# Kernel optimization log

Measured on AMD Instinct MI355X. Metric: run time of the kernel, lower is better.

Reference implementation:

```python
import jax, jax.numpy as jnp
import numpy as np

D_MODEL = 1024
N_SA = 8          # self-attention heads
N_RA = 8          # relational-attention heads
TOTAL = N_SA + N_RA
HEAD_DIM = D_MODEL // TOTAL   # 64
KEY_DIM = HEAD_DIM            # default key_dim = d_model // total_n_heads
N_REL = 8                     # n_relations (= n_heads_ra default)
REL_PROJ = KEY_DIM            # rel_proj_dim default
B, S = 4, 1024


def _rope(x, cos, sin):
    # x: [b, s, h, d]; cos/sin: [s, d//2]; interleaved-pair rotation as in apply_rotary_emb
    xr = x.reshape(x.shape[:-1] + (-1, 2))
    x_r, x_i = xr[..., 0], xr[..., 1]
    c = cos[None, :, None, :]
    s = sin[None, :, None, :]
    o_r = x_r * c - x_i * s
    o_i = x_r * s + x_i * c
    return jnp.stack([o_r, o_i], axis=-1).reshape(x.shape)


def setup_inputs() -> dict:
    key = jax.random.key(0)
    ks = jax.random.split(key, 16)
    def p(k, shape, scale=0.02):
        return jax.random.normal(k, shape, dtype=jnp.float32) * scale
    x = jax.random.normal(ks[0], (B, S, D_MODEL), dtype=jnp.float32)
    symbols = jax.random.normal(ks[1], (B, S, D_MODEL), dtype=jnp.float32)
    # standard RoPE frequency tables, shape [S, KEY_DIM//2]
    inv_freq = 1.0 / (10000.0 ** (np.arange(0, KEY_DIM, 2, dtype=np.float32) / KEY_DIM))
    ang = np.outer(np.arange(S, dtype=np.float32), inv_freq)
    freqs_cos = jnp.asarray(np.cos(ang), dtype=jnp.float32)
    freqs_sin = jnp.asarray(np.sin(ang), dtype=jnp.float32)
    return dict(
        x=x, symbols=symbols, freqs_cos=freqs_cos, freqs_sin=freqs_sin,
        # self-attention stream params
        wq_sa=p(ks[2], (D_MODEL, N_SA * KEY_DIM)),
        wk_sa=p(ks[3], (D_MODEL, N_SA * KEY_DIM)),
        wv_sa=p(ks[4], (D_MODEL, N_SA * HEAD_DIM)),
        wo_sa=p(ks[5], (N_SA * HEAD_DIM, N_SA * HEAD_DIM)),
        # relational-attention stream params
        wq_attn=p(ks[6], (D_MODEL, N_RA * KEY_DIM)),
        wk_attn=p(ks[7], (D_MODEL, N_RA * KEY_DIM)),
        wq_rel=p(ks[8], (D_MODEL, N_REL * REL_PROJ)),
        wk_rel=p(ks[9], (D_MODEL, N_REL * REL_PROJ)),
        wr=p(ks[10], (N_RA, HEAD_DIM, N_REL)),      # per-head relation->head_dim map
        wv_sym=p(ks[11], (D_MODEL, N_RA * HEAD_DIM)),  # symbol projection
        wo_ra=p(ks[12], (N_RA * HEAD_DIM, N_RA * HEAD_DIM)),
    )


def reference(x, symbols, freqs_cos, freqs_sin, wq_sa, wk_sa, wv_sa, wo_sa,
              wq_attn, wk_attn, wq_rel, wk_rel, wr, wv_sym, wo_ra):
    b, s, _ = x.shape
    attn_scale = 1.0 / jnp.sqrt(jnp.asarray(HEAD_DIM, dtype=x.dtype))
    rel_scale = 1.0 / jnp.sqrt(jnp.asarray(REL_PROJ, dtype=x.dtype))
    causal = jnp.tril(jnp.ones((s, s), dtype=bool))
    neg = jnp.where(causal, jnp.asarray(0.0, x.dtype), jnp.asarray(-jnp.inf, x.dtype))

    # ---- standard self-attention stream ----
    q = _rope((x @ wq_sa).reshape(b, s, N_SA, KEY_DIM), freqs_cos, freqs_sin)
    k = _rope((x @ wk_sa).reshape(b, s, N_SA, KEY_DIM), freqs_cos, freqs_sin)
    v = (x @ wv_sa).reshape(b, s, N_SA, HEAD_DIM)
    scores = jnp.einsum('bihd,bjhd->bhij', q, k) * attn_scale + neg
    attn = jax.nn.softmax(scores, axis=-1)
    sa_out = jnp.einsum('bhij,bjhd->bihd', attn, v).reshape(b, s, -1) @ wo_sa

    # ---- relational attention stream ----
    qa = _rope((x @ wq_attn).reshape(b, s, N_RA, KEY_DIM), freqs_cos, freqs_sin)
    ka = _rope((x @ wk_attn).reshape(b, s, N_RA, KEY_DIM), freqs_cos, freqs_sin)
    ra_scores = jnp.einsum('bihd,bjhd->bhij', qa, ka) * attn_scale + neg
    ra_attn = jax.nn.softmax(ra_scores, axis=-1)
    # relations r(i,j) in R^{n_rel}: inner products of relation projections, tanh-activated
    qr = (x @ wq_rel).reshape(b, s, N_REL, REL_PROJ)
    kr = (x @ wk_rel).reshape(b, s, N_REL, REL_PROJ)
    rel = jnp.tanh(jnp.einsum('bird,bjrd->bijr', qr, kr) * rel_scale)  # [b,s,s,n_rel]
    sv = (symbols @ wv_sym).reshape(b, s, N_RA, HEAD_DIM)
    sym_msg = jnp.einsum('bhij,bjhd->bihd', ra_attn, sv)
    rel_msg = jnp.einsum('bhij,bijr->bihr', ra_attn, rel)
    rel_proj = jnp.einsum('bihr,hdr->bihd', rel_msg, wr)
    ra_out = (sym_msg + rel_proj).reshape(b, s, -1) @ wo_ra

    # dual attention: concat the two streams along feature dim -> [b, s, d_model]
    return jnp.concatenate([sa_out, ra_out], axis=-1)
```

## Files before the change

### kernel.cpp

```cpp
#include <hip/hip_runtime.h>

typedef unsigned short u16;
typedef unsigned int u32;
typedef __attribute__((ext_vector_type(8))) short s16x8;
typedef __attribute__((ext_vector_type(4))) float f32x4;

#define C_QSA 0
#define C_KSA 512
#define C_VSA 1024
#define C_QA  1536
#define C_KA  2048
#define C_QR  2560
#define C_KR  3072
#define C_SV  3584
#define LDP   4096

__device__ __forceinline__ u16 f2bf(float f) {
    union { float f; unsigned u; } v; v.f = f;
    return (u16)((v.u + 0x7FFFu + ((v.u >> 16) & 1u)) >> 16);
}
__device__ __forceinline__ float bf2f(u16 h) {
    union { unsigned u; float f; } v; v.u = ((unsigned)h) << 16; return v.f;
}
__device__ __forceinline__ float fexp(float y) {
    return __builtin_exp2f(y * 1.4426950408889634f);
}
__device__ __forceinline__ float ftanh(float x) {
    float e = __builtin_exp2f(x * 2.885390081777927f);
    return 1.f - 2.f / (e + 1.f);
}
__device__ __forceinline__ f32x4 mfma16(s16x8 a, s16x8 b, f32x4 c) {
    return __builtin_amdgcn_mfma_f32_16x16x32_bf16(a, b, c, 0, 0, 0);
}
__device__ __forceinline__ void gload16(const u16* g, u16* l) {
    __builtin_amdgcn_global_load_lds(
        (const __attribute__((address_space(1))) void*)g,
        (__attribute__((address_space(3))) void*)l, 16, 0, 0);
}


__global__ void cvt2_f32_bf16(const float* __restrict__ a, const float* __restrict__ b,
                              u16* __restrict__ oa, u16* __restrict__ ob) {
    int i = (blockIdx.x * 256 + threadIdx.x) * 8;
    const int half = (i >= 4194304) ? 1 : 0;
    const float* in = half ? b : a;
    u16* out = half ? ob : oa;
    int off = i - half * 4194304;
    float4 x = *(const float4*)(in + off);
    float4 y = *(const float4*)(in + off + 4);
    s16x8 o;
    o[0] = (short)f2bf(x.x); o[1] = (short)f2bf(x.y);
    o[2] = (short)f2bf(x.z); o[3] = (short)f2bf(x.w);
    o[4] = (short)f2bf(y.x); o[5] = (short)f2bf(y.y);
    o[6] = (short)f2bf(y.z); o[7] = (short)f2bf(y.w);
    *(s16x8*)(out + off) = o;
}

struct WP { const float* p[10]; };

__global__ void transpose_w(WP wp, u16* __restrict__ WcatT,
                            u16* __restrict__ woSaT, u16* __restrict__ woRaT) {
    const int z = blockIdx.z;
    const float* W;
    u16* Wt;
    int K;
    if (z < 8) { W = wp.p[z]; Wt = WcatT + (size_t)z * 524288; K = 1024; }
    else       { W = wp.p[z]; Wt = (z == 8) ? woSaT : woRaT;   K = 512;  }
    const int N = 512;
    const int kt = blockIdx.x * 32, nt = blockIdx.y * 32;
    if (kt >= K) return;
    __shared__ float t[32][33];
    const int c = threadIdx.x & 31, r0 = threadIdx.x >> 5;
#pragma unroll
    for (int it = 0; it < 4; ++it) {
        int r = it * 8 + r0;
        t[r][c] = W[(size_t)(kt + r) * N + nt + c];
    }
    __syncthreads();
#pragma unroll
    for (int it = 0; it < 4; ++it) {
        int r = it * 8 + r0;
        Wt[(size_t)(nt + r) * K + kt + c] = f2bf(t[c][r]);
    }
}

__global__ void transpose_v2(const u16* __restrict__ P, u16* __restrict__ Vt, int colOff) {
    const int st = blockIdx.x * 32, ht = blockIdx.y * 32, b = blockIdx.z;
    __shared__ u16 t[32][34];
    const int c = threadIdx.x & 31, r0 = threadIdx.x >> 5;
#pragma unroll
    for (int it = 0; it < 4; ++it) {
        int r = it * 8 + r0;
        t[r][c] = P[(size_t)(b * 1024 + st + r) * LDP + colOff + ht + c];
    }
    __syncthreads();
    const int cp = ((c & 15) >> 2) * 8 + (c >> 4) * 4 + (c & 3);
#pragma unroll
    for (int it = 0; it < 4; ++it) {
        int r = it * 8 + r0;
        Vt[(size_t)b * 524288 + (size_t)(ht + r) * 1024 + st + cp] = t[c][r];
    }
}


__global__ void rope_kernel(u16* __restrict__ P, const float* __restrict__ fcos,
                            const float* __restrict__ fsin) {
    int idx = blockIdx.x * 256 + threadIdx.x;
    int row = idx >> 10;
    int rem = idx & 1023;
    int region = rem >> 8;
    int pr = rem & 255;
    int head = pr >> 5, p = pr & 31;
    int off = (region + (region >> 1)) * 512;
    int col = off + head * 64 + 2 * p;
    int s = row & 1023;
    float c = fcos[s * 32 + p], sn = fsin[s * 32 + p];
    u32* ptr = (u32*)(P + (size_t)row * LDP + col);
    u32 v = *ptr;
    float xr = bf2f((u16)(v & 0xffff)), xi = bf2f((u16)(v >> 16));
    u16 o0 = f2bf(xr * c - xi * sn);
    u16 o1 = f2bf(xr * sn + xi * c);
    *ptr = (u32)o0 | ((u32)o1 << 16);
}


template<bool OUT_BF16, bool SWZ>
__global__ __launch_bounds__(256) void gemm_bf16(
    const u16* __restrict__ A, const u16* __restrict__ A2, int lda, int nswitch,
    const u16* __restrict__ Bt, int ldb,
    void* __restrict__ Cp, int ldc, int ccolOff, int K)
{
    __shared__ u16 As[128][64];
    __shared__ u16 Bs[128][64];
    const int tid = threadIdx.x;
    int bx = blockIdx.x, by = blockIdx.y;
    if (SWZ) {
        int lin = by * gridDim.x + bx;
        int k = lin & 7, j = lin >> 3;
        bx = (k & 3) * 8 + (j & 7);
        by = (k >> 2) * 16 + (j >> 3);
    }
    const int m0 = bx * 128, n0 = by * 128;
    const u16* Ause = (A2 != nullptr && n0 >= nswitch) ? A2 : A;
    const int w = tid >> 6, lane = tid & 63;
    const int w32 = w * 32;
    const int wm = (w >> 1) * 64, wn = (w & 1) * 64;
    const int lr = lane & 15, lg = lane >> 4;
    const int srow = lane >> 3;
    const int sc16 = ((lane & 7) ^ srow) * 8;
    f32x4 acc[4][4] = {};

    for (int k0 = 0; k0 < K; k0 += 64) {
        const u16* ga = &Ause[(size_t)(m0 + w32 + srow) * lda + k0 + sc16];
        const u16* gb = &Bt [(size_t)(n0 + w32 + srow) * ldb + k0 + sc16];
        gload16(ga,            &As[w32][0]);
        gload16(ga +  8 * lda, &As[w32 +  8][0]);
        gload16(ga + 16 * lda, &As[w32 + 16][0]);
        gload16(ga + 24 * lda, &As[w32 + 24][0]);
        gload16(gb,            &Bs[w32][0]);
        gload16(gb +  8 * ldb, &Bs[w32 +  8][0]);
        gload16(gb + 16 * ldb, &Bs[w32 + 16][0]);
        gload16(gb + 24 * ldb, &Bs[w32 + 24][0]);
        __syncthreads();
#pragma unroll
        for (int kk = 0; kk < 2; ++kk) {
            s16x8 af[4], bfr[4];
#pragma unroll
            for (int t = 0; t < 4; ++t) {
                const int ca = (((kk * 4 + lg) ^ (lr & 7)) * 8);
                af[t]  = *(const s16x8*)&As[wm + t * 16 + lr][ca];
                bfr[t] = *(const s16x8*)&Bs[wn + t * 16 + lr][ca];
            }
#pragma unroll
            for (int i = 0; i < 4; ++i)
#pragma unroll
                for (int j = 0; j < 4; ++j)
                    acc[i][j] = mfma16(af[i], bfr[j], acc[i][j]);
        }
        __syncthreads();
    }
#pragma unroll
    for (int i = 0; i < 4; ++i)
#pragma unroll
        for (int j = 0; j < 4; ++j)
#pragma unroll
            for (int r = 0; r < 4; ++r) {
                int row = m0 + wm + i * 16 + lg * 4 + r;
                int col = n0 + wn + j * 16 + lr;
                float val = acc[i][j][r];
                if (OUT_BF16)
                    ((u16*)Cp)[(size_t)row * ldc + ccolOff + col] = f2bf(val);
                else
                    ((float*)Cp)[(size_t)row * ldc + ccolOff + col] = val;
            }
}


__global__ __launch_bounds__(64) void attn_sa(u16* __restrict__ P, const u16* __restrict__ Vt) {
    const int bid = blockIdx.x;
    const int h = bid & 7;
    const int b = (bid >> 3) & 3;
    const int pr = bid >> 5;
    const int xt1 = pr, xt2 = 63 - pr;
    const int lane = threadIdx.x, lr = lane & 15, lg = lane >> 4;
    const size_t rowBase = (size_t)b * 1024;
    const int i0_1 = xt1 * 16, i0_2 = xt2 * 16;
    const int ir1 = i0_1 + lr, ir2 = i0_2 + lr;

    const u16* Kbase = P + rowBase * LDP + (C_KSA + h * 64);
    const u16* Vb = Vt + ((size_t)(b * 8 + h)) * 65536;

    s16x8 q1[2], q2[2];
    {
        const u16* q = P + (rowBase + ir1) * LDP + (C_QSA + h * 64) + lg * 8;
        q1[0] = *(const s16x8*)q; q1[1] = *(const s16x8*)(q + 32);
        q = P + (rowBase + ir2) * LDP + (C_QSA + h * 64) + lg * 8;
        q2[0] = *(const s16x8*)q; q2[1] = *(const s16x8*)(q + 32);
    }
    f32x4 o1[4] = {}, o2[4] = {};
    float l1 = 0.f, l2 = 0.f;
    const int njt  = (xt2 >> 1) + 1;
    const int njt1 = (xt1 >> 1) + 1;

    for (int jt = 0; jt < njt; ++jt) {
        const int j0 = jt * 32;
        const bool act1 = (jt < njt1);
        s16x8 kf[2][2], vfr[4];
#pragma unroll
        for (int sub = 0; sub < 2; ++sub) {
            const u16* kp = Kbase + (size_t)(j0 + sub * 16 + lr) * LDP + lg * 8;
            kf[sub][0] = *(const s16x8*)kp;
            kf[sub][1] = *(const s16x8*)(kp + 32);
        }
#pragma unroll
        for (int ds = 0; ds < 4; ++ds)
            vfr[ds] = *(const s16x8*)(Vb + (size_t)(ds * 16 + lr) * 1024 + j0 + 8 * lg);

        f32x4 sc2[2] = {{0.f,0.f,0.f,0.f},{0.f,0.f,0.f,0.f}};
        f32x4 sc1[2] = {{0.f,0.f,0.f,0.f},{0.f,0.f,0.f,0.f}};
#pragma unroll
        for (int sub = 0; sub < 2; ++sub) {
            sc2[sub] = mfma16(kf[sub][0], q2[0], sc2[sub]);
            sc2[sub] = mfma16(kf[sub][1], q2[1], sc2[sub]);
        }
        if (act1) {
#pragma unroll
            for (int sub = 0; sub < 2; ++sub) {
                sc1[sub] = mfma16(kf[sub][0], q1[0], sc1[sub]);
                sc1[sub] = mfma16(kf[sub][1], q1[1], sc1[sub]);
            }
        }
        s16x8 pa;
#pragma unroll
        for (int sub = 0; sub < 2; ++sub)
#pragma unroll
            for (int r = 0; r < 4; ++r) {
                int j = j0 + sub * 16 + 4 * lg + r;
                float p = (j <= ir2) ? fexp(sc2[sub][r] * 0.125f) : 0.f;
                l2 += p;
                pa[sub * 4 + r] = (short)f2bf(p);
            }
#pragma unroll
        for (int ds = 0; ds < 4; ++ds) o2[ds] = mfma16(pa, vfr[ds], o2[ds]);
        if (act1) {
#pragma unroll
            for (int sub = 0; sub < 2; ++sub)
#pragma unroll
                for (int r = 0; r < 4; ++r) {
                    int j = j0 + sub * 16 + 4 * lg + r;
                    float p = (j <= ir1) ? fexp(sc1[sub][r] * 0.125f) : 0.f;
                    l1 += p;
                    pa[sub * 4 + r] = (short)f2bf(p);
                }
#pragma unroll
            for (int ds = 0; ds < 4; ++ds) o1[ds] = mfma16(pa, vfr[ds], o1[ds]);
        }
    }
    l1 += __shfl_xor(l1, 16); l1 += __shfl_xor(l1, 32);
    l2 += __shfl_xor(l2, 16); l2 += __shfl_xor(l2, 32);
    float li1[4], li2[4];
#pragma unroll
    for (int r = 0; r < 4; ++r) {
        li1[r] = 1.f / __shfl(l1, 4 * lg + r);
        li2[r] = 1.f / __shfl(l2, 4 * lg + r);
    }
#pragma unroll
    for (int ds = 0; ds < 4; ++ds)
#pragma unroll
        for (int r = 0; r < 4; ++r) {
            P[(rowBase + i0_1 + 4 * lg + r) * LDP + (C_QSA + h * 64) + ds * 16 + lr] =
                f2bf(o1[ds][r] * li1[r]);
            P[(rowBase + i0_2 + 4 * lg + r) * LDP + (C_QSA + h * 64) + ds * 16 + lr] =
                f2bf(o2[ds][r] * li2[r]);
        }
}


__global__ __launch_bounds__(512) void attn_ra(u16* __restrict__ P, const u16* __restrict__ SVt,
                                               float* __restrict__ opart,
                                               float* __restrict__ mlr) {
    const int bid = blockIdx.x;
    const int slot = bid & 7;
    const int b = slot & 3, s = slot >> 2;
    const int xt = 63 - (bid >> 3);
    const int w = threadIdx.x >> 6, lane = threadIdx.x & 63;
    const int lr = lane & 15, lg = lane >> 4;
    const int h = w;
    const size_t rowBase = (size_t)b * 1024;
    const int i0 = xt * 16;
    const int ir = i0 + lr;

    __shared__ float relT[2][2][32][16][8];

    const u16* Kbase  = P + rowBase * LDP + (C_KA + h * 64);
    const u16* KRbase = P + rowBase * LDP + (C_KR + h * 64);
    const u16* Vb = SVt + ((size_t)(b * 8 + h)) * 65536;

    s16x8 qf[2], qrf[2];
    {
        const u16* q = P + (rowBase + ir) * LDP + (C_QA + h * 64) + lg * 8;
        qf[0] = *(const s16x8*)q; qf[1] = *(const s16x8*)(q + 32);
        const u16* qr = P + (rowBase + ir) * LDP + (C_QR + h * 64) + lg * 8;
        qrf[0] = *(const s16x8*)qr; qrf[1] = *(const s16x8*)(qr + 32);
    }
    f32x4 o[4] = {};
    float rmr[8] = {};
    float l = 0.f;
    const int njt = (xt >> 1) + 1;
    const int cnt = (njt - s + 1) >> 1;
    const int npair = (cnt + 1) >> 1;
    const int slotw = (w + lr) & 7;

    for (int u = 0; u < npair; ++u) {
        const int j0a = (s + 4 * u) * 32;
        const bool actB = (2 * u + 1) < cnt;
        const int j0b = actB ? j0a + 64 : j0a;
        s16x8 kfA[2][2], krA[2][2], kfB[2][2], krB[2][2], vfA[4], vfB[4];
#pragma unroll
        for (int sub = 0; sub < 2; ++sub) {
            const u16* kp = Kbase + (size_t)(j0a + sub * 16 + lr) * LDP + lg * 8;
            kfA[sub][0] = *(const s16x8*)kp;  kfA[sub][1] = *(const s16x8*)(kp + 32);
            const u16* krp = KRbase + (size_t)(j0a + sub * 16 + lr) * LDP + lg * 8;
            krA[sub][0] = *(const s16x8*)krp; krA[sub][1] = *(const s16x8*)(krp + 32);
            kp = Kbase + (size_t)(j0b + sub * 16 + lr) * LDP + lg * 8;
            kfB[sub][0] = *(const s16x8*)kp;  kfB[sub][1] = *(const s16x8*)(kp + 32);
            krp = KRbase + (size_t)(j0b + sub * 16 + lr) * LDP + lg * 8;
            krB[sub][0] = *(const s16x8*)krp; krB[sub][1] = *(const s16x8*)(krp + 32);
        }
#pragma unroll
        for (int ds = 0; ds < 4; ++ds) {
            vfA[ds] = *(const s16x8*)(Vb + (size_t)(ds * 16 + lr) * 1024 + j0a + 8 * lg);
            vfB[ds] = *(const s16x8*)(Vb + (size_t)(ds * 16 + lr) * 1024 + j0b + 8 * lg);
        }
        f32x4 scA[2] = {{0.f,0.f,0.f,0.f},{0.f,0.f,0.f,0.f}};
        f32x4 scB[2] = {{0.f,0.f,0.f,0.f},{0.f,0.f,0.f,0.f}};
        f32x4 rtA[2] = {{0.f,0.f,0.f,0.f},{0.f,0.f,0.f,0.f}};
        f32x4 rtB[2] = {{0.f,0.f,0.f,0.f},{0.f,0.f,0.f,0.f}};
#pragma unroll
        for (int sub = 0; sub < 2; ++sub) {
            scA[sub] = mfma16(kfA[sub][0], qf[0], scA[sub]);
            scA[sub] = mfma16(kfA[sub][1], qf[1], scA[sub]);
            rtA[sub] = mfma16(krA[sub][0], qrf[0], rtA[sub]);
            rtA[sub] = mfma16(krA[sub][1], qrf[1], rtA[sub]);
            scB[sub] = mfma16(kfB[sub][0], qf[0], scB[sub]);
            scB[sub] = mfma16(kfB[sub][1], qf[1], scB[sub]);
            rtB[sub] = mfma16(krB[sub][0], qrf[0], rtB[sub]);
            rtB[sub] = mfma16(krB[sub][1], qrf[1], rtB[sub]);
        }
        float pA[2][4], pB[2][4];
#pragma unroll
        for (int sub = 0; sub < 2; ++sub)
#pragma unroll
            for (int r = 0; r < 4; ++r) {
                int jA = j0a + sub * 16 + 4 * lg + r;
                int jB = j0b + sub * 16 + 4 * lg + r;
                pA[sub][r] = (jA <= ir) ? fexp(scA[sub][r] * 0.125f) : 0.f;
                pB[sub][r] = (actB && jB <= ir) ? fexp(scB[sub][r] * 0.125f) : 0.f;
                l += pA[sub][r] + pB[sub][r];
            }
#pragma unroll
        for (int sub = 0; sub < 2; ++sub)
#pragma unroll
            for (int r = 0; r < 4; ++r) {
                int jp = sub * 16 + 4 * lg + r;
                relT[u & 1][0][jp][lr][slotw] = ftanh(rtA[sub][r] * 0.125f);
                relT[u & 1][1][jp][lr][slotw] = ftanh(rtB[sub][r] * 0.125f);
            }
        __syncthreads();
#pragma unroll
        for (int sub = 0; sub < 2; ++sub)
#pragma unroll
            for (int r = 0; r < 4; ++r) {
                int jp = sub * 16 + 4 * lg + r;
                f32x4 a  = *(const f32x4*)&relT[u & 1][0][jp][lr][0];
                f32x4 bb = *(const f32x4*)&relT[u & 1][0][jp][lr][4];
                float pv = pA[sub][r];
#pragma unroll
                for (int k = 0; k < 4; ++k) {
                    rmr[k]     += pv * a[k];
                    rmr[4 + k] += pv * bb[k];
                }
                a  = *(const f32x4*)&relT[u & 1][1][jp][lr][0];
                bb = *(const f32x4*)&relT[u & 1][1][jp][lr][4];
                pv = pB[sub][r];
#pragma unroll
                for (int k = 0; k < 4; ++k) {
                    rmr[k]     += pv * a[k];
                    rmr[4 + k] += pv * bb[k];
                }
            }
        s16x8 paA, paB;
#pragma unroll
        for (int r = 0; r < 4; ++r) {
            paA[r]     = (short)f2bf(pA[0][r]);
            paA[4 + r] = (short)f2bf(pA[1][r]);
            paB[r]     = (short)f2bf(pB[0][r]);
            paB[4 + r] = (short)f2bf(pB[1][r]);
        }
#pragma unroll
        for (int ds = 0; ds < 4; ++ds) {
            o[ds] = mfma16(paA, vfA[ds], o[ds]);
            o[ds] = mfma16(paB, vfB[ds], o[ds]);
        }
    }

    l += __shfl_xor(l, 16); l += __shfl_xor(l, 32);
#pragma unroll
    for (int k = 0; k < 8; ++k) {
        float v = rmr[k];
        v += __shfl_xor(v, 16);
        v += __shfl_xor(v, 32);
        rmr[k] = v;
    }
    float g[8], t0[8];
    const int t = lr & 7;
#pragma unroll
    for (int k = 0; k < 8; ++k) g[k] = rmr[k];
#pragma unroll
    for (int k = 0; k < 8; ++k) t0[k] = (t & 1) ? g[(k + 1) & 7] : g[k];
#pragma unroll
    for (int k = 0; k < 8; ++k) g[k]  = (t & 2) ? t0[(k + 2) & 7] : t0[k];
#pragma unroll
    for (int k = 0; k < 8; ++k) t0[k] = (t & 4) ? g[(k + 4) & 7] : g[k];

    const int headRow = (b * 8 + h) * 1024;
#pragma unroll
    for (int ds = 0; ds < 4; ++ds)
#pragma unroll
        for (int r = 0; r < 4; ++r) {
            int row = headRow + i0 + 4 * lg + r;
            opart[((size_t)row * 2 + s) * 64 + ds * 16 + lr] = o[ds][r];
        }
    if (lg == 0) {
        float* pm = &mlr[((size_t)(headRow + i0 + lr) * 2 + s) * 10];
        pm[0] = l;
#pragma unroll
        for (int c = 0; c < 8; ++c) pm[1 + c] = t0[c];
    }
}


__global__ __launch_bounds__(256) void merge_ra(const float* __restrict__ opart,
                                                const float* __restrict__ mlr,
                                                const float* __restrict__ wr,
                                                u16* __restrict__ P) {
    const int gid = blockIdx.x * 4 + (threadIdx.x >> 6);
    const int d = threadIdx.x & 63;
    const int i = gid & 1023;
    const int h = (gid >> 10) & 7;
    const int b = gid >> 13;
    const float* ml0 = &mlr[(size_t)gid * 20];
    const float* ml1 = ml0 + 10;
    float ilt = 1.f / (ml0[0] + ml1[0]);
    float acc = (opart[(size_t)gid * 128 + d] +
                 opart[(size_t)gid * 128 + 64 + d]) * ilt;
#pragma unroll
    for (int c = 0; c < 8; ++c) {
        float rm = (ml0[1 + c] + ml1[1 + c]) * ilt;
        acc += rm * wr[h * 512 + d * 8 + c];
    }
    P[((size_t)(b * 1024 + i)) * LDP + C_QA + h * 64 + d] = f2bf(acc);
}


extern "C" void kernel_launch(void* const* d_in, const int* in_sizes, int n_in,
                              void* d_out, int out_size, void* d_ws, size_t ws_size,
                              hipStream_t stream)
{
    const float* x     = (const float*)d_in[0];
    const float* sym   = (const float*)d_in[1];
    const float* fcos  = (const float*)d_in[2];
    const float* fsin  = (const float*)d_in[3];
    const float* w_qsa = (const float*)d_in[4];
    const float* w_ksa = (const float*)d_in[5];
    const float* w_vsa = (const float*)d_in[6];
    const float* w_osa = (const float*)d_in[7];
    const float* w_qa  = (const float*)d_in[8];
    const float* w_ka  = (const float*)d_in[9];
    const float* w_qr  = (const float*)d_in[10];
    const float* w_kr  = (const float*)d_in[11];
    const float* wr    = (const float*)d_in[12];
    const float* w_sv  = (const float*)d_in[13];
    const float* w_ora = (const float*)d_in[14];

    char* ws = (char*)d_ws;
    u16* xb    = (u16*)(ws);
    u16* symb  = (u16*)(ws + (8u  << 20));
    u16* WcatT = (u16*)(ws + (16u << 20));
    u16* woSaT = (u16*)(ws + (24u << 20));
    u16* woRaT = (u16*)(ws + (24u << 20) + (512u << 10));
    u16* Pcat  = (u16*)(ws + (25u << 20));
    u16* vT    = (u16*)(ws + (57u << 20));
    u16* svT   = (u16*)(ws + (61u << 20));
    float* opart = (float*)(ws);
    float* mlrp  = (float*)(ws + (17u << 20));

    cvt2_f32_bf16<<<4096, 256, 0, stream>>>(x, sym, xb, symb);

    WP wp{{w_qsa, w_ksa, w_vsa, w_qa, w_ka, w_qr, w_kr, w_sv, w_osa, w_ora}};
    transpose_w<<<dim3(32, 16, 10), 256, 0, stream>>>(wp, WcatT, woSaT, woRaT);

    gemm_bf16<true, true><<<dim3(32, 32), 256, 0, stream>>>(
        xb, symb, 1024, C_SV, WcatT, 1024, Pcat, LDP, 0, 1024);

    rope_kernel<<<16384, 256, 0, stream>>>(Pcat, fcos, fsin);

    transpose_v2<<<dim3(32, 16, 4), 256, 0, stream>>>(Pcat, vT,  C_VSA);
    transpose_v2<<<dim3(32, 16, 4), 256, 0, stream>>>(Pcat, svT, C_SV);

    attn_sa<<<1024, 64, 0, stream>>>(Pcat, vT);
    attn_ra<<<512, 512, 0, stream>>>(Pcat, svT, opart, mlrp);
    merge_ra<<<8192, 256, 0, stream>>>(opart, mlrp, wr, Pcat);

    gemm_bf16<false, false><<<dim3(32, 8), 256, 0, stream>>>(
        Pcat + C_QSA, Pcat + C_QA, LDP, 512, woSaT, 512, d_out, 1024, 0, 512);
}
```

Before: 202.5 us.

## Fuse self-attention into relational attention kernel and merge both streams together

Removes the standalone self-attention kernel and computes it inside the relational attention kernel, reusing the same block and key-split layout, so both streams share one launch and one merge pass. The two V transposes are merged into a single launch, and the partial outputs are stored as bf16 instead of fp32 to cut workspace traffic. The cost is higher register pressure in the combined kernel (launch bounds now request 4 blocks) and extra rounding from writing the partial sums in bf16.

```diff
diff --git a/kernel.cpp b/kernel.cpp
--- a/kernel.cpp
+++ b/kernel.cpp
@@ -84,8 +84,13 @@
     }
 }
 
-__global__ void transpose_v2(const u16* __restrict__ P, u16* __restrict__ Vt, int colOff) {
-    const int st = blockIdx.x * 32, ht = blockIdx.y * 32, b = blockIdx.z;
+__global__ void transpose_v2(const u16* __restrict__ P, u16* __restrict__ vT,
+                             u16* __restrict__ svT) {
+    const int st = blockIdx.x * 32, ht = blockIdx.y * 32;
+    const int z = blockIdx.z;
+    const int b = z & 3;
+    const int colOff = (z < 4) ? C_VSA : C_SV;
+    u16* Vt = (z < 4) ? vT : svT;
     __shared__ u16 t[32][34];
     const int c = threadIdx.x & 31, r0 = threadIdx.x >> 5;
 #pragma unroll
@@ -196,109 +201,11 @@
 }
 
 
-__global__ __launch_bounds__(64) void attn_sa(u16* __restrict__ P, const u16* __restrict__ Vt) {
-    const int bid = blockIdx.x;
-    const int h = bid & 7;
-    const int b = (bid >> 3) & 3;
-    const int pr = bid >> 5;
-    const int xt1 = pr, xt2 = 63 - pr;
-    const int lane = threadIdx.x, lr = lane & 15, lg = lane >> 4;
-    const size_t rowBase = (size_t)b * 1024;
-    const int i0_1 = xt1 * 16, i0_2 = xt2 * 16;
-    const int ir1 = i0_1 + lr, ir2 = i0_2 + lr;
-
-    const u16* Kbase = P + rowBase * LDP + (C_KSA + h * 64);
-    const u16* Vb = Vt + ((size_t)(b * 8 + h)) * 65536;
-
-    s16x8 q1[2], q2[2];
-    {
-        const u16* q = P + (rowBase + ir1) * LDP + (C_QSA + h * 64) + lg * 8;
-        q1[0] = *(const s16x8*)q; q1[1] = *(const s16x8*)(q + 32);
-        q = P + (rowBase + ir2) * LDP + (C_QSA + h * 64) + lg * 8;
-        q2[0] = *(const s16x8*)q; q2[1] = *(const s16x8*)(q + 32);
-    }
-    f32x4 o1[4] = {}, o2[4] = {};
-    float l1 = 0.f, l2 = 0.f;
-    const int njt  = (xt2 >> 1) + 1;
-    const int njt1 = (xt1 >> 1) + 1;
-
-    for (int jt = 0; jt < njt; ++jt) {
-        const int j0 = jt * 32;
-        const bool act1 = (jt < njt1);
-        s16x8 kf[2][2], vfr[4];
-#pragma unroll
-        for (int sub = 0; sub < 2; ++sub) {
-            const u16* kp = Kbase + (size_t)(j0 + sub * 16 + lr) * LDP + lg * 8;
-            kf[sub][0] = *(const s16x8*)kp;
-            kf[sub][1] = *(const s16x8*)(kp + 32);
-        }
-#pragma unroll
-        for (int ds = 0; ds < 4; ++ds)
-            vfr[ds] = *(const s16x8*)(Vb + (size_t)(ds * 16 + lr) * 1024 + j0 + 8 * lg);
-
-        f32x4 sc2[2] = {{0.f,0.f,0.f,0.f},{0.f,0.f,0.f,0.f}};
-        f32x4 sc1[2] = {{0.f,0.f,0.f,0.f},{0.f,0.f,0.f,0.f}};
-#pragma unroll
-        for (int sub = 0; sub < 2; ++sub) {
-            sc2[sub] = mfma16(kf[sub][0], q2[0], sc2[sub]);
-            sc2[sub] = mfma16(kf[sub][1], q2[1], sc2[sub]);
-        }
-        if (act1) {
-#pragma unroll
-            for (int sub = 0; sub < 2; ++sub) {
-                sc1[sub] = mfma16(kf[sub][0], q1[0], sc1[sub]);
-                sc1[sub] = mfma16(kf[sub][1], q1[1], sc1[sub]);
-            }
-        }
-        s16x8 pa;
-#pragma unroll
-        for (int sub = 0; sub < 2; ++sub)
-#pragma unroll
-            for (int r = 0; r < 4; ++r) {
-                int j = j0 + sub * 16 + 4 * lg + r;
-                float p = (j <= ir2) ? fexp(sc2[sub][r] * 0.125f) : 0.f;
-                l2 += p;
-                pa[sub * 4 + r] = (short)f2bf(p);
-            }
-#pragma unroll
-        for (int ds = 0; ds < 4; ++ds) o2[ds] = mfma16(pa, vfr[ds], o2[ds]);
-        if (act1) {
-#pragma unroll
-            for (int sub = 0; sub < 2; ++sub)
-#pragma unroll
-                for (int r = 0; r < 4; ++r) {
-                    int j = j0 + sub * 16 + 4 * lg + r;
-                    float p = (j <= ir1) ? fexp(sc1[sub][r] * 0.125f) : 0.f;
-                    l1 += p;
-                    pa[sub * 4 + r] = (short)f2bf(p);
-                }
-#pragma unroll
-            for (int ds = 0; ds < 4; ++ds) o1[ds] = mfma16(pa, vfr[ds], o1[ds]);
-        }
-    }
-    l1 += __shfl_xor(l1, 16); l1 += __shfl_xor(l1, 32);
-    l2 += __shfl_xor(l2, 16); l2 += __shfl_xor(l2, 32);
-    float li1[4], li2[4];
-#pragma unroll
-    for (int r = 0; r < 4; ++r) {
-        li1[r] = 1.f / __shfl(l1, 4 * lg + r);
-        li2[r] = 1.f / __shfl(l2, 4 * lg + r);
-    }
-#pragma unroll
-    for (int ds = 0; ds < 4; ++ds)
-#pragma unroll
-        for (int r = 0; r < 4; ++r) {
-            P[(rowBase + i0_1 + 4 * lg + r) * LDP + (C_QSA + h * 64) + ds * 16 + lr] =
-                f2bf(o1[ds][r] * li1[r]);
-            P[(rowBase + i0_2 + 4 * lg + r) * LDP + (C_QSA + h * 64) + ds * 16 + lr] =
-                f2bf(o2[ds][r] * li2[r]);
-        }
-}
-
-
-__global__ __launch_bounds__(512) void attn_ra(u16* __restrict__ P, const u16* __restrict__ SVt,
-                                               float* __restrict__ opart,
-                                               float* __restrict__ mlr) {
+__global__ __launch_bounds__(512, 4) void attn_both(
+    u16* __restrict__ P, const u16* __restrict__ Vt, const u16* __restrict__ SVt,
+    u16* __restrict__ opRA, float* __restrict__ mlrRA,
+    u16* __restrict__ opSA, float* __restrict__ lSA)
+{
     const int bid = blockIdx.x;
     const int slot = bid & 7;
     const int b = slot & 3, s = slot >> 2;
@@ -314,18 +221,22 @@
 
     const u16* Kbase  = P + rowBase * LDP + (C_KA + h * 64);
     const u16* KRbase = P + rowBase * LDP + (C_KR + h * 64);
-    const u16* Vb = SVt + ((size_t)(b * 8 + h)) * 65536;
-
-    s16x8 qf[2], qrf[2];
+    const u16* KSbase = P + rowBase * LDP + (C_KSA + h * 64);
+    const u16* Vb  = SVt + ((size_t)(b * 8 + h)) * 65536;
+    const u16* Vsb = Vt  + ((size_t)(b * 8 + h)) * 65536;
+
+    s16x8 qf[2], qrf[2], qs[2];
     {
         const u16* q = P + (rowBase + ir) * LDP + (C_QA + h * 64) + lg * 8;
         qf[0] = *(const s16x8*)q; qf[1] = *(const s16x8*)(q + 32);
         const u16* qr = P + (rowBase + ir) * LDP + (C_QR + h * 64) + lg * 8;
         qrf[0] = *(const s16x8*)qr; qrf[1] = *(const s16x8*)(qr + 32);
-    }
-    f32x4 o[4] = {};
+        const u16* qq = P + (rowBase + ir) * LDP + (C_QSA + h * 64) + lg * 8;
+        qs[0] = *(const s16x8*)qq; qs[1] = *(const s16x8*)(qq + 32);
+    }
+    f32x4 o[4] = {}, os[4] = {};
     float rmr[8] = {};
-    float l = 0.f;
+    float l = 0.f, ls = 0.f;
     const int njt = (xt >> 1) + 1;
     const int cnt = (njt - s + 1) >> 1;
     const int npair = (cnt + 1) >> 1;
@@ -335,96 +246,132 @@
         const int j0a = (s + 4 * u) * 32;
         const bool actB = (2 * u + 1) < cnt;
         const int j0b = actB ? j0a + 64 : j0a;
-        s16x8 kfA[2][2], krA[2][2], kfB[2][2], krB[2][2], vfA[4], vfB[4];
-#pragma unroll
-        for (int sub = 0; sub < 2; ++sub) {
-            const u16* kp = Kbase + (size_t)(j0a + sub * 16 + lr) * LDP + lg * 8;
-            kfA[sub][0] = *(const s16x8*)kp;  kfA[sub][1] = *(const s16x8*)(kp + 32);
-            const u16* krp = KRbase + (size_t)(j0a + sub * 16 + lr) * LDP + lg * 8;
-            krA[sub][0] = *(const s16x8*)krp; krA[sub][1] = *(const s16x8*)(krp + 32);
-            kp = Kbase + (size_t)(j0b + sub * 16 + lr) * LDP + lg * 8;
-            kfB[sub][0] = *(const s16x8*)kp;  kfB[sub][1] = *(const s16x8*)(kp + 32);
-            krp = KRbase + (size_t)(j0b + sub * 16 + lr) * LDP + lg * 8;
-            krB[sub][0] = *(const s16x8*)krp; krB[sub][1] = *(const s16x8*)(krp + 32);
+        {
+            s16x8 kfA[2][2], krA[2][2], kfB[2][2], krB[2][2], vfA[4], vfB[4];
+#pragma unroll
+            for (int sub = 0; sub < 2; ++sub) {
+                const u16* kp = Kbase + (size_t)(j0a + sub * 16 + lr) * LDP + lg * 8;
+                kfA[sub][0] = *(const s16x8*)kp;  kfA[sub][1] = *(const s16x8*)(kp + 32);
+                const u16* krp = KRbase + (size_t)(j0a + sub * 16 + lr) * LDP + lg * 8;
+                krA[sub][0] = *(const s16x8*)krp; krA[sub][1] = *(const s16x8*)(krp + 32);
+                kp = Kbase + (size_t)(j0b + sub * 16 + lr) * LDP + lg * 8;
+                kfB[sub][0] = *(const s16x8*)kp;  kfB[sub][1] = *(const s16x8*)(kp + 32);
+                krp = KRbase + (size_t)(j0b + sub * 16 + lr) * LDP + lg * 8;
+                krB[sub][0] = *(const s16x8*)krp; krB[sub][1] = *(const s16x8*)(krp + 32);
+            }
+#pragma unroll
+            for (int ds = 0; ds < 4; ++ds) {
+                vfA[ds] = *(const s16x8*)(Vb + (size_t)(ds * 16 + lr) * 1024 + j0a + 8 * lg);
+                vfB[ds] = *(const s16x8*)(Vb + (size_t)(ds * 16 + lr) * 1024 + j0b + 8 * lg);
+            }
+            f32x4 scA[2] = {{0.f,0.f,0.f,0.f},{0.f,0.f,0.f,0.f}};
+            f32x4 scB[2] = {{0.f,0.f,0.f,0.f},{0.f,0.f,0.f,0.f}};
+            f32x4 rtA[2] = {{0.f,0.f,0.f,0.f},{0.f,0.f,0.f,0.f}};
+            f32x4 rtB[2] = {{0.f,0.f,0.f,0.f},{0.f,0.f,0.f,0.f}};
+#pragma unroll
+            for (int sub = 0; sub < 2; ++sub) {
+                scA[sub] = mfma16(kfA[sub][0], qf[0], scA[sub]);
+                scA[sub] = mfma16(kfA[sub][1], qf[1], scA[sub]);
+                rtA[sub] = mfma16(krA[sub][0], qrf[0], rtA[sub]);
+                rtA[sub] = mfma16(krA[sub][1], qrf[1], rtA[sub]);
+                scB[sub] = mfma16(kfB[sub][0], qf[0], scB[sub]);
+                scB[sub] = mfma16(kfB[sub][1], qf[1], scB[sub]);
+                rtB[sub] = mfma16(krB[sub][0], qrf[0], rtB[sub]);
+                rtB[sub] = mfma16(krB[sub][1], qrf[1], rtB[sub]);
+            }
+            float pA[2][4], pB[2][4];
+#pragma unroll
+            for (int sub = 0; sub < 2; ++sub)
+#pragma unroll
+                for (int r = 0; r < 4; ++r) {
+                    int jA = j0a + sub * 16 + 4 * lg + r;
+                    int jB = j0b + sub * 16 + 4 * lg + r;
+                    pA[sub][r] = (jA <= ir) ? fexp(scA[sub][r] * 0.125f) : 0.f;
+                    pB[sub][r] = (actB && jB <= ir) ? fexp(scB[sub][r] * 0.125f) : 0.f;
+                    l += pA[sub][r] + pB[sub][r];
+                }
+#pragma unroll
+            for (int sub = 0; sub < 2; ++sub)
+#pragma unroll
+                for (int r = 0; r < 4; ++r) {
+                    int jp = sub * 16 + 4 * lg + r;
+                    relT[u & 1][0][jp][lr][slotw] = ftanh(rtA[sub][r] * 0.125f);
+                    relT[u & 1][1][jp][lr][slotw] = ftanh(rtB[sub][r] * 0.125f);
+                }
+            __syncthreads();
+#pragma unroll
+            for (int sub = 0; sub < 2; ++sub)
+#pragma unroll
+                for (int r = 0; r < 4; ++r) {
+                    int jp = sub * 16 + 4 * lg + r;
+                    f32x4 a  = *(const f32x4*)&relT[u & 1][0][jp][lr][0];
+                    f32x4 bb = *(const f32x4*)&relT[u & 1][0][jp][lr][4];
+                    float pv = pA[sub][r];
+#pragma unroll
+                    for (int k = 0; k < 4; ++k) {
+                        rmr[k]     += pv * a[k];
+                        rmr[4 + k] += pv * bb[k];
+                    }
+                    a  = *(const f32x4*)&relT[u & 1][1][jp][lr][0];
+                    bb = *(const f32x4*)&relT[u & 1][1][jp][lr][4];
+                    pv = pB[sub][r];
+#pragma unroll
+                    for (int k = 0; k < 4; ++k) {
+                        rmr[k]     += pv * a[k];
+                        rmr[4 + k] += pv * bb[k];
+                    }
+                }
+            s16x8 paA, paB;
+#pragma unroll
+            for (int r = 0; r < 4; ++r) {
+                paA[r]     = (short)f2bf(pA[0][r]);
+                paA[4 + r] = (short)f2bf(pA[1][r]);
+                paB[r]     = (short)f2bf(pB[0][r]);
+                paB[4 + r] = (short)f2bf(pB[1][r]);
+            }
+#pragma unroll
+            for (int ds = 0; ds < 4; ++ds) {
+                o[ds] = mfma16(paA, vfA[ds], o[ds]);
+                o[ds] = mfma16(paB, vfB[ds], o[ds]);
+            }
         }
 #pragma unroll
-        for (int ds = 0; ds < 4; ++ds) {
-            vfA[ds] = *(const s16x8*)(Vb + (size_t)(ds * 16 + lr) * 1024 + j0a + 8 * lg);
-            vfB[ds] = *(const s16x8*)(Vb + (size_t)(ds * 16 + lr) * 1024 + j0b + 8 * lg);
+        for (int tb = 0; tb < 2; ++tb) {
+            if (tb == 1 && !actB) break;
+            const int j0 = tb ? j0b : j0a;
+            s16x8 ks[2][2], vs[4];
+#pragma unroll
+            for (int sub = 0; sub < 2; ++sub) {
+                const u16* kp = KSbase + (size_t)(j0 + sub * 16 + lr) * LDP + lg * 8;
+                ks[sub][0] = *(const s16x8*)kp;
+                ks[sub][1] = *(const s16x8*)(kp + 32);
+            }
+#pragma unroll
+            for (int ds = 0; ds < 4; ++ds)
+                vs[ds] = *(const s16x8*)(Vsb + (size_t)(ds * 16 + lr) * 1024 + j0 + 8 * lg);
+            f32x4 sc[2] = {{0.f,0.f,0.f,0.f},{0.f,0.f,0.f,0.f}};
+#pragma unroll
+            for (int sub = 0; sub < 2; ++sub) {
+                sc[sub] = mfma16(ks[sub][0], qs[0], sc[sub]);
+                sc[sub] = mfma16(ks[sub][1], qs[1], sc[sub]);
+            }
+            s16x8 pa;
+#pragma unroll
+            for (int sub = 0; sub < 2; ++sub)
+#pragma unroll
+                for (int r = 0; r < 4; ++r) {
+                    int j = j0 + sub * 16 + 4 * lg + r;
+                    float p = (j <= ir) ? fexp(sc[sub][r] * 0.125f) : 0.f;
+                    ls += p;
+                    pa[sub * 4 + r] = (short)f2bf(p);
+                }
+#pragma unroll
+            for (int ds = 0; ds < 4; ++ds) os[ds] = mfma16(pa, vs[ds], os[ds]);
         }
-        f32x4 scA[2] = {{0.f,0.f,0.f,0.f},{0.f,0.f,0.f,0.f}};
-        f32x4 scB[2] = {{0.f,0.f,0.f,0.f},{0.f,0.f,0.f,0.f}};
-        f32x4 rtA[2] = {{0.f,0.f,0.f,0.f},{0.f,0.f,0.f,0.f}};
-        f32x4 rtB[2] = {{0.f,0.f,0.f,0.f},{0.f,0.f,0.f,0.f}};
-#pragma unroll
-        for (int sub = 0; sub < 2; ++sub) {
-            scA[sub] = mfma16(kfA[sub][0], qf[0], scA[sub]);
-            scA[sub] = mfma16(kfA[sub][1], qf[1], scA[sub]);
-            rtA[sub] = mfma16(krA[sub][0], qrf[0], rtA[sub]);
-            rtA[sub] = mfma16(krA[sub][1], qrf[1], rtA[sub]);
-            scB[sub] = mfma16(kfB[sub][0], qf[0], scB[sub]);
-            scB[sub] = mfma16(kfB[sub][1], qf[1], scB[sub]);
-            rtB[sub] = mfma16(krB[sub][0], qrf[0], rtB[sub]);
-            rtB[sub] = mfma16(krB[sub][1], qrf[1], rtB[sub]);
-        }
-        float pA[2][4], pB[2][4];
-#pragma unroll
-        for (int sub = 0; sub < 2; ++sub)
-#pragma unroll
-            for (int r = 0; r < 4; ++r) {
-                int jA = j0a + sub * 16 + 4 * lg + r;
-                int jB = j0b + sub * 16 + 4 * lg + r;
-                pA[sub][r] = (jA <= ir) ? fexp(scA[sub][r] * 0.125f) : 0.f;
-                pB[sub][r] = (actB && jB <= ir) ? fexp(scB[sub][r] * 0.125f) : 0.f;
-                l += pA[sub][r] + pB[sub][r];
-            }
-#pragma unroll
-        for (int sub = 0; sub < 2; ++sub)
-#pragma unroll
-            for (int r = 0; r < 4; ++r) {
-                int jp = sub * 16 + 4 * lg + r;
-                relT[u & 1][0][jp][lr][slotw] = ftanh(rtA[sub][r] * 0.125f);
-                relT[u & 1][1][jp][lr][slotw] = ftanh(rtB[sub][r] * 0.125f);
-            }
-        __syncthreads();
-#pragma unroll
-        for (int sub = 0; sub < 2; ++sub)
-#pragma unroll
-            for (int r = 0; r < 4; ++r) {
-                int jp = sub * 16 + 4 * lg + r;
-                f32x4 a  = *(const f32x4*)&relT[u & 1][0][jp][lr][0];
-                f32x4 bb = *(const f32x4*)&relT[u & 1][0][jp][lr][4];
-                float pv = pA[sub][r];
-#pragma unroll
-                for (int k = 0; k < 4; ++k) {
-                    rmr[k]     += pv * a[k];
-                    rmr[4 + k] += pv * bb[k];
-                }
-                a  = *(const f32x4*)&relT[u & 1][1][jp][lr][0];
-                bb = *(const f32x4*)&relT[u & 1][1][jp][lr][4];
-                pv = pB[sub][r];
-#pragma unroll
-                for (int k = 0; k < 4; ++k) {
-                    rmr[k]     += pv * a[k];
-                    rmr[4 + k] += pv * bb[k];
-                }
-            }
-        s16x8 paA, paB;
-#pragma unroll
-        for (int r = 0; r < 4; ++r) {
-            paA[r]     = (short)f2bf(pA[0][r]);
-            paA[4 + r] = (short)f2bf(pA[1][r]);
-            paB[r]     = (short)f2bf(pB[0][r]);
-            paB[4 + r] = (short)f2bf(pB[1][r]);
-        }
-#pragma unroll
-        for (int ds = 0; ds < 4; ++ds) {
-            o[ds] = mfma16(paA, vfA[ds], o[ds]);
-            o[ds] = mfma16(paB, vfB[ds], o[ds]);
-        }
-    }
-
-    l += __shfl_xor(l, 16); l += __shfl_xor(l, 32);
+    }
+
+    l  += __shfl_xor(l, 16);  l  += __shfl_xor(l, 32);
+    ls += __shfl_xor(ls, 16); ls += __shfl_xor(ls, 32);
 #pragma unroll
     for (int k = 0; k < 8; ++k) {
         float v = rmr[k];
@@ -449,37 +396,44 @@
 #pragma unroll
         for (int r = 0; r < 4; ++r) {
             int row = headRow + i0 + 4 * lg + r;
-            opart[((size_t)row * 2 + s) * 64 + ds * 16 + lr] = o[ds][r];
+            opRA[((size_t)row * 2 + s) * 64 + ds * 16 + lr] = f2bf(o[ds][r]);
+            opSA[((size_t)row * 2 + s) * 64 + ds * 16 + lr] = f2bf(os[ds][r]);
         }
     if (lg == 0) {
-        float* pm = &mlr[((size_t)(headRow + i0 + lr) * 2 + s) * 10];
+        float* pm = &mlrRA[((size_t)(headRow + i0 + lr) * 2 + s) * 9];
         pm[0] = l;
 #pragma unroll
         for (int c = 0; c < 8; ++c) pm[1 + c] = t0[c];
-    }
-}
-
-
-__global__ __launch_bounds__(256) void merge_ra(const float* __restrict__ opart,
-                                                const float* __restrict__ mlr,
-                                                const float* __restrict__ wr,
-                                                u16* __restrict__ P) {
+        lSA[(size_t)(headRow + i0 + lr) * 2 + s] = ls;
+    }
+}
+
+
+__global__ __launch_bounds__(256) void merge_both(
+    const u16* __restrict__ opRA, const float* __restrict__ mlrRA,
+    const u16* __restrict__ opSA, const float* __restrict__ lSA,
+    const float* __restrict__ wr, u16* __restrict__ P)
+{
     const int gid = blockIdx.x * 4 + (threadIdx.x >> 6);
     const int d = threadIdx.x & 63;
     const int i = gid & 1023;
     const int h = (gid >> 10) & 7;
     const int b = gid >> 13;
-    const float* ml0 = &mlr[(size_t)gid * 20];
-    const float* ml1 = ml0 + 10;
+    const float* ml0 = &mlrRA[(size_t)gid * 18];
+    const float* ml1 = ml0 + 9;
     float ilt = 1.f / (ml0[0] + ml1[0]);
-    float acc = (opart[(size_t)gid * 128 + d] +
-                 opart[(size_t)gid * 128 + 64 + d]) * ilt;
+    float acc = (bf2f(opRA[(size_t)gid * 128 + d]) +
+                 bf2f(opRA[(size_t)gid * 128 + 64 + d])) * ilt;
 #pragma unroll
     for (int c = 0; c < 8; ++c) {
         float rm = (ml0[1 + c] + ml1[1 + c]) * ilt;
         acc += rm * wr[h * 512 + d * 8 + c];
     }
     P[((size_t)(b * 1024 + i)) * LDP + C_QA + h * 64 + d] = f2bf(acc);
+    float ilts = 1.f / (lSA[(size_t)gid * 2] + lSA[(size_t)gid * 2 + 1]);
+    float accs = (bf2f(opSA[(size_t)gid * 128 + d]) +
+                  bf2f(opSA[(size_t)gid * 128 + 64 + d])) * ilts;
+    P[((size_t)(b * 1024 + i)) * LDP + C_QSA + h * 64 + d] = f2bf(accs);
 }
 
 
@@ -512,8 +466,10 @@
     u16* Pcat  = (u16*)(ws + (25u << 20));
     u16* vT    = (u16*)(ws + (57u << 20));
     u16* svT   = (u16*)(ws + (61u << 20));
-    float* opart = (float*)(ws);
-    float* mlrp  = (float*)(ws + (17u << 20));
+    u16*   opRA  = (u16*)(ws);
+    u16*   opSA  = (u16*)(ws + (9u  << 20));
+    float* mlrRA = (float*)(ws + (18u << 20));
+    float* lSAp  = (float*)(ws + (21u << 20));
 
     cvt2_f32_bf16<<<4096, 256, 0, stream>>>(x, sym, xb, symb);
 
@@ -525,12 +481,10 @@
 
     rope_kernel<<<16384, 256, 0, stream>>>(Pcat, fcos, fsin);
 
-    transpose_v2<<<dim3(32, 16, 4), 256, 0, stream>>>(Pcat, vT,  C_VSA);
-    transpose_v2<<<dim3(32, 16, 4), 256, 0, stream>>>(Pcat, svT, C_SV);
-
-    attn_sa<<<1024, 64, 0, stream>>>(Pcat, vT);
-    attn_ra<<<512, 512, 0, stream>>>(Pcat, svT, opart, mlrp);
-    merge_ra<<<8192, 256, 0, stream>>>(opart, mlrp, wr, Pcat);
+    transpose_v2<<<dim3(32, 16, 8), 256, 0, stream>>>(Pcat, vT, svT);
+
+    attn_both<<<512, 512, 0, stream>>>(Pcat, vT, svT, opRA, mlrRA, opSA, lSAp);
+    merge_both<<<8192, 256, 0, stream>>>(opRA, mlrRA, opSA, lSAp, wr, Pcat);
 
     gemm_bf16<false, false><<<dim3(32, 8), 256, 0, stream>>>(
         Pcat + C_QSA, Pcat + C_QA, LDP, 512, woSaT, 512, d_out, 1024, 0, 512);
```

Result: slower. 427.0 us (+110.8%).
